# Kernel optimization log

Measured on AMD Instinct MI355X. Metric: run time of the kernel, lower is better.

Reference implementation:

```python
import jax, jax.numpy as jnp
import numpy as np

B, S, D, H = 2, 2048, 1024, 16
DK = D // H

def setup_inputs() -> dict:
    key = jax.random.key(0)
    ks = jax.random.split(key, 11)
    scale = 1.0 / np.sqrt(D)
    inp = {
        'q': jax.random.normal(ks[0], (B, S, D), jnp.float32),
        'k': jax.random.normal(ks[1], (B, S, D), jnp.float32),
        'v': jax.random.normal(ks[2], (B, S, D), jnp.float32),
        'mask': jnp.ones((1, 1, S, S), jnp.int32),
        'Wq': jax.random.normal(ks[3], (D, D), jnp.float32) * scale,
        'bq': jnp.zeros((D,), jnp.float32),
        'Wk': jax.random.normal(ks[4], (D, D), jnp.float32) * scale,
        'bk': jnp.zeros((D,), jnp.float32),
        'Wv': jax.random.normal(ks[5], (D, D), jnp.float32) * scale,
        'bv': jnp.zeros((D,), jnp.float32),
        'Wo': jax.random.normal(ks[6], (D, D), jnp.float32) * scale,
        'bo': jnp.zeros((D,), jnp.float32),
    }
    return inp

def reference(q, k, v, mask, Wq, bq, Wk, bk, Wv, bv, Wo, bo):
    # Linear projections, split into heads: [B,S,D] -> [B,H,S,DK]
    def proj(x, W, b):
        return (x @ W + b).reshape(B, -1, H, DK).transpose(0, 2, 1, 3)
    Q = proj(q, Wq, bq)
    K = proj(k, Wk, bk)
    V = proj(v, Wv, bv)
    scores = jnp.einsum('bhqd,bhkd->bhqk', Q, K) / jnp.sqrt(jnp.float32(DK))
    scores = jnp.where(mask == 0, jnp.float32(-1e9), scores)
    attn = jax.nn.softmax(scores, axis=-1)  # dropout is identity in eval mode
    out = jnp.einsum('bhqk,bhkd->bhqd', attn, V)
    out = out.transpose(0, 2, 1, 3).reshape(B, -1, D)
    return out @ Wo + bo
```

## Files before the change

### kernel.cpp

```cpp
#include <hip/hip_runtime.h>
#include <stdint.h>

#define B_  2
#define S_  2048
#define D_  1024
#define H_  16
#define M_  (B_*S_)

typedef __attribute__((ext_vector_type(8)))  short  short8;
typedef __attribute__((ext_vector_type(4)))  float  floatx4;
typedef __attribute__((ext_vector_type(16))) float  floatx16;
typedef __attribute__((ext_vector_type(4)))  float  f32x4;
typedef __attribute__((ext_vector_type(8)))  unsigned short u16x8;
typedef __attribute__((ext_vector_type(4)))  unsigned short u16x4;
typedef __attribute__((ext_vector_type(2)))  unsigned int   uint2v;

#define LOG2E_  1.44269504088896f
#define QSCALE_ (0.125f * LOG2E_)

#if __has_builtin(__builtin_amdgcn_exp2f)
  #define EXP2(x) __builtin_amdgcn_exp2f(x)
#else
  #define EXP2(x) exp2f(x)
#endif

__device__ __forceinline__ unsigned short f2bf(float x){
  union { float f; uint32_t u; } v; v.f = x;
  uint32_t r = v.u + 0x7FFFu + ((v.u >> 16) & 1u);
  return (unsigned short)(r >> 16);
}

__device__ __forceinline__ uint32_t cvt_pk_bf16(float lo, float hi){
  uint32_t r;
  asm("v_cvt_pk_bf16_f32 %0, %1, %2" : "=v"(r) : "v"(lo), "v"(hi));
  return r;
}

__device__ __forceinline__ void pl32swap(uint32_t &a, uint32_t &b){
#if __has_builtin(__builtin_amdgcn_permlane32_swap)
  uint2v r = __builtin_amdgcn_permlane32_swap(a, b, false, false);
  a = r[0]; b = r[1];
#else
  const int hi = (threadIdx.x & 63) >> 5;
  uint32_t sa = (uint32_t)__shfl_xor((int)a, 32);
  uint32_t sb = (uint32_t)__shfl_xor((int)b, 32);
  uint32_t na = hi ? sb : a;
  uint32_t nb = hi ? b  : sa;
  a = na; b = nb;
#endif
}

#define GLL16(G, L) __builtin_amdgcn_global_load_lds( \
    (const __attribute__((address_space(1))) void*)(G), \
    (__attribute__((address_space(3))) void*)(L), 16, 0, 0)

__global__ __launch_bounds__(256) void k_cvt3(const float* __restrict__ q,
        const float* __restrict__ k, const float* __restrict__ v,
        unsigned short* __restrict__ qb, unsigned short* __restrict__ kb,
        unsigned short* __restrict__ vb){
  const int z = blockIdx.y;
  const float* src = z==0 ? q : z==1 ? k : v;
  unsigned short* dst = z==0 ? qb : z==1 ? kb : vb;
  int i = blockIdx.x*256 + threadIdx.x;
  f32x4 a = ((const f32x4*)src)[i*2];
  f32x4 b = ((const f32x4*)src)[i*2+1];
  u16x8 o;
  o[0]=f2bf(a[0]); o[1]=f2bf(a[1]); o[2]=f2bf(a[2]); o[3]=f2bf(a[3]);
  o[4]=f2bf(b[0]); o[5]=f2bf(b[1]); o[6]=f2bf(b[2]); o[7]=f2bf(b[3]);
  ((u16x8*)dst)[i] = o;
}

__global__ __launch_bounds__(256) void k_wt4(const float* __restrict__ Wq,
        const float* __restrict__ Wk, const float* __restrict__ Wv, const float* __restrict__ Wo,
        unsigned short* __restrict__ wqt, unsigned short* __restrict__ wkt,
        unsigned short* __restrict__ wvt, unsigned short* __restrict__ wot){
  const int z = blockIdx.z;
  const float* W = z==0 ? Wq : z==1 ? Wk : z==2 ? Wv : Wo;
  unsigned short* Wt = z==0 ? wqt : z==1 ? wkt : z==2 ? wvt : wot;
  __shared__ float tile[32][33];
  int n0 = blockIdx.x*32, k0 = blockIdx.y*32;
  int tx = threadIdx.x, ty = threadIdx.y;
  #pragma unroll
  for (int i=0;i<32;i+=8) tile[ty+i][tx] = W[(size_t)(k0+ty+i)*D_ + n0+tx];
  __syncthreads();
  #pragma unroll
  for (int i=0;i<32;i+=8) Wt[(size_t)(n0+ty+i)*D_ + k0+tx] = f2bf(tile[tx][ty+i]);
}

__global__ __launch_bounds__(256) void k_vt64(const unsigned short* __restrict__ Vp,
                                              unsigned short* __restrict__ Vt){
  __shared__ __align__(16) unsigned short t[64*72];
  const int tid = threadIdx.x;
  const int col0 = blockIdx.x*64, row0 = blockIdx.y*64;
  const int b = row0 >> 11, s0 = row0 & 2047;
  #pragma unroll
  for (int it=0; it<2; ++it){
    int i = it*256 + tid;
    int r = i >> 3, c = i & 7;
    short8 v8 = *(const short8*)(Vp + (size_t)(row0 + r)*D_ + col0 + c*8);
    #pragma unroll
    for (int j=0;j<8;j++){
      int d = c*8 + j;
      t[d*72 + (((r>>3) ^ (d&7))*8) + (r&7)] = (unsigned short)v8[j];
    }
  }
  __syncthreads();
  #pragma unroll
  for (int it=0; it<2; ++it){
    int i = it*256 + tid;
    int d = i >> 3, c = i & 7;
    short8 v8 = *(const short8*)(t + d*72 + ((c ^ (d&7))*8));
    *(short8*)(Vt + (size_t)(b*1024 + col0 + d)*S_ + s0 + c*8) = v8;
  }
}

__global__ __launch_bounds__(256) void k_gemm_qkv(
        const unsigned short* __restrict__ qb, const unsigned short* __restrict__ kb,
        const unsigned short* __restrict__ vb,
        const unsigned short* __restrict__ wqt, const unsigned short* __restrict__ wkt,
        const unsigned short* __restrict__ wvt,
        const float* __restrict__ bq, const float* __restrict__ bk, const float* __restrict__ bv,
        unsigned short* __restrict__ Qp, unsigned short* __restrict__ Kp,
        unsigned short* __restrict__ Vp)
{
  __shared__ __align__(16) unsigned short As[128*32];
  __shared__ __align__(16) unsigned short Bs[128*32];
  const int z = blockIdx.z;
  const unsigned short* A  = z==0 ? qb  : z==1 ? kb  : vb;
  const unsigned short* Bt = z==0 ? wqt : z==1 ? wkt : wvt;
  const float* bias        = z==0 ? bq  : z==1 ? bk  : bv;
  unsigned short* C        = z==0 ? Qp  : z==1 ? Kp  : Vp;
  const float scale        = z==0 ? QSCALE_ : 1.0f;

  const int tid = threadIdx.x;
  const int lane = tid & 63, wid = tid >> 6;
  const int wr = wid >> 1, wc = wid & 1;
  const int row0 = blockIdx.y*128, col0 = blockIdx.x*128;
  const int l15 = lane & 15, l4 = lane >> 4;

  floatx4 acc[4][4];
  #pragma unroll
  for (int i=0;i<4;i++)
    #pragma unroll
    for (int j=0;j<4;j++)
      #pragma unroll
      for (int r=0;r<4;r++) acc[i][j][r] = 0.f;

  for (int k0=0; k0<D_; k0+=32){
    __syncthreads();
    #pragma unroll
    for (int it=0; it<2; it++){
      int idx = it*256 + tid;
      int r = idx >> 2, c = idx & 3;
      GLL16(A  + (size_t)(row0 + r)*D_ + k0 + c*8, As + (size_t)(it*4 + wid)*512);
      GLL16(Bt + (size_t)(col0 + r)*D_ + k0 + c*8, Bs + (size_t)(it*4 + wid)*512);
    }
    __syncthreads();
    short8 af[4], bfr[4];
    #pragma unroll
    for (int i=0;i<4;i++)
      af[i] = *(const short8*)(As + (wr*64 + i*16 + l15)*32 + l4*8);
    #pragma unroll
    for (int j=0;j<4;j++)
      bfr[j] = *(const short8*)(Bs + (wc*64 + j*16 + l15)*32 + l4*8);
    #pragma unroll
    for (int i=0;i<4;i++)
      #pragma unroll
      for (int j=0;j<4;j++)
        acc[i][j] = __builtin_amdgcn_mfma_f32_16x16x32_bf16(af[i], bfr[j], acc[i][j], 0,0,0);
  }

  #pragma unroll
  for (int i=0;i<4;i++){
    #pragma unroll
    for (int j=0;j<4;j++){
      int col = col0 + wc*64 + j*16 + l15;
      float bv_ = bias[col];
      int rowb = row0 + wr*64 + i*16 + l4*4;
      #pragma unroll
      for (int r=0;r<4;r++)
        C[(size_t)(rowb + r)*D_ + col] = f2bf((acc[i][j][r] + bv_) * scale);
    }
  }
}

__global__ __launch_bounds__(256) void k_gemm_out(const unsigned short* __restrict__ A,
        const unsigned short* __restrict__ Bt, const float* __restrict__ bias,
        float* __restrict__ C)
{
  __shared__ __align__(16) unsigned short smem[12288];
  unsigned short* const As0 = smem;
  unsigned short* const Bs0 = smem + 2048;
  unsigned short* const As1 = smem + 6144;
  unsigned short* const Bs1 = smem + 8192;

  const int bid = blockIdx.x;
  const int xcd = bid & 7, i2 = bid >> 3;
  const int row0 = (xcd + (i2 >> 3)*8) * 64, col0 = (i2 & 7) * 128;

  const int tid = threadIdx.x;
  const int lane = tid & 63, wid = tid >> 6;
  const int l15 = lane & 15, l4 = lane >> 4;

  floatx4 acc[4][2];
  #pragma unroll
  for (int i=0;i<4;i++)
    #pragma unroll
    for (int j=0;j<2;j++)
      #pragma unroll
      for (int r=0;r<4;r++) acc[i][j][r] = 0.f;

  auto STAGE = [&](unsigned short* As, unsigned short* Bs, int k0){
    #pragma unroll
    for (int it=0; it<2; it++){
      int idx = it*256 + tid;
      int r = idx >> 2, c = idx & 3;
      GLL16(Bt + (size_t)(col0 + r)*D_ + k0 + c*8, Bs + (size_t)(it*4 + wid)*512);
    }
    {
      int r = tid >> 2, c = tid & 3;
      GLL16(A + (size_t)(row0 + r)*D_ + k0 + c*8, As + (size_t)wid*512);
    }
  };
  auto COMPUTE = [&](const unsigned short* As, const unsigned short* Bs){
    short8 af[4], bfr[2];
    #pragma unroll
    for (int i=0;i<4;i++)
      af[i] = *(const short8*)(As + (i*16 + l15)*32 + l4*8);
    #pragma unroll
    for (int j=0;j<2;j++)
      bfr[j] = *(const short8*)(Bs + (wid*32 + j*16 + l15)*32 + l4*8);
    #pragma unroll
    for (int i=0;i<4;i++)
      #pragma unroll
      for (int j=0;j<2;j++)
        acc[i][j] = __builtin_amdgcn_mfma_f32_16x16x32_bf16(af[i], bfr[j], acc[i][j], 0,0,0);
  };

  STAGE(As0, Bs0, 0);
  __syncthreads();
  #pragma unroll 1
  for (int k0=0; k0<D_; k0+=64){
    STAGE(As1, Bs1, k0+32);
    COMPUTE(As0, Bs0);
    __syncthreads();
    if (k0 + 64 < D_) STAGE(As0, Bs0, k0+64);
    COMPUTE(As1, Bs1);
    __syncthreads();
  }

  #pragma unroll
  for (int i=0;i<4;i++){
    #pragma unroll
    for (int j=0;j<2;j++){
      int col = col0 + wid*32 + j*16 + l15;
      float bv_ = bias[col];
      int rowb = row0 + i*16 + l4*4;
      #pragma unroll
      for (int r=0;r<4;r++)
        C[(size_t)(rowb + r)*D_ + col] = acc[i][j][r] + bv_;
    }
  }
}

__global__ __launch_bounds__(256,4) void k_attn(const unsigned short* __restrict__ Qp,
        const unsigned short* __restrict__ Kp, const unsigned short* __restrict__ Vt,
        float* __restrict__ Op, float* __restrict__ Lp)
{
  __shared__ __align__(16) unsigned short smem[16384];
  unsigned short* const kb0 = smem;
  unsigned short* const vb0 = smem + 4096;
  unsigned short* const kb1 = smem + 8192;
  unsigned short* const vb1 = smem + 12288;

  const int sblk = blockIdx.x;
  const int xcd = sblk & 7, jj = sblk >> 3;
  const int bh = xcd + 8*(jj >> 5);
  const int rem = jj & 31, qt = rem >> 1, part = rem & 1;
  const int b = bh >> 4, h = bh & 15;
  const int q0 = qt*128;

  const int tid  = threadIdx.x;
  const int lane = tid & 63, wid = tid >> 6;
  const int lo5  = lane & 31, hi = lane >> 5;
  const int qm = b*S_ + q0 + wid*32 + lo5;

  short8 qf[4];
  #pragma unroll
  for (int f=0; f<4; f++)
    qf[f] = *(const short8*)(Qp + (size_t)qm*D_ + h*64 + f*16 + hi*8);

  floatx16 zv;
  #pragma unroll
  for (int r=0;r<16;r++) zv[r] = 0.f;
  floatx16 ot0 = zv, ot1 = zv;
  float lsum = 0.f;

  const int srow = tid >> 3;
  const int sc   = (tid & 7) ^ (srow & 7);
  const unsigned short* kp0 = Kp + ((size_t)b*S_)*D_ + h*64
                              + (size_t)(part*1024 + srow)*D_ + sc*8;
  const unsigned short* kp1 = kp0 + (size_t)32*D_;
  const unsigned short* vp0 = Vt + ((size_t)(b*1024 + h*64 + srow))*S_ + part*1024 + sc*8;
  const unsigned short* vp1 = vp0 + (size_t)32*S_;

  auto STAGE = [&](unsigned short* kdst, unsigned short* vdst, int tt){
    const size_t ko = (size_t)tt*64*D_;
    const int    vo = tt*64;
    GLL16(kp0 + ko, kdst + wid*512);
    GLL16(kp1 + ko, kdst + (4+wid)*512);
    GLL16(vp0 + vo, vdst + wid*512);
    GLL16(vp1 + vo, vdst + (4+wid)*512);
  };

  const int ksw = lo5 & 7;

  auto COMPUTE = [&](const unsigned short* kbuf, const unsigned short* vbuf){
    floatx16 st0, st1;
    __builtin_amdgcn_s_setprio(1);
    {
      const int cc = hi ^ ksw;
      short8 ka0 = *(const short8*)(kbuf + lo5*64      + cc*8);
      short8 ka1 = *(const short8*)(kbuf + (32+lo5)*64 + cc*8);
      st0 = __builtin_amdgcn_mfma_f32_32x32x16_bf16(ka0, qf[0], zv, 0,0,0);
      st1 = __builtin_amdgcn_mfma_f32_32x32x16_bf16(ka1, qf[0], zv, 0,0,0);
    }
    #pragma unroll
    for (int f=1; f<4; f++){
      const int cc = (2*f + hi) ^ ksw;
      short8 ka0 = *(const short8*)(kbuf + lo5*64      + cc*8);
      short8 ka1 = *(const short8*)(kbuf + (32+lo5)*64 + cc*8);
      st0 = __builtin_amdgcn_mfma_f32_32x32x16_bf16(ka0, qf[f], st0, 0,0,0);
      st1 = __builtin_amdgcn_mfma_f32_32x32x16_bf16(ka1, qf[f], st1, 0,0,0);
    }
    __builtin_amdgcn_s_setprio(0);

    #pragma unroll
    for (int kh=0; kh<2; kh++){
      const floatx16& st = kh ? st1 : st0;
      #pragma unroll
      for (int blk=0; blk<2; blk++){
        const int bs = blk*8;
        float e0 = EXP2(st[bs+0]), e1 = EXP2(st[bs+1]);
        float e2 = EXP2(st[bs+2]), e3 = EXP2(st[bs+3]);
        float e4 = EXP2(st[bs+4]), e5 = EXP2(st[bs+5]);
        float e6 = EXP2(st[bs+6]), e7 = EXP2(st[bs+7]);
        lsum += ((e0+e1)+(e2+e3)) + ((e4+e5)+(e6+e7));
        uint32_t a01 = cvt_pk_bf16(e0,e1);
        uint32_t a23 = cvt_pk_bf16(e2,e3);
        uint32_t a45 = cvt_pk_bf16(e4,e5);
        uint32_t a67 = cvt_pk_bf16(e6,e7);
        pl32swap(a01, a45);
        pl32swap(a23, a67);
        union { uint32_t w[4]; short8 v; } pu;
        pu.w[0] = a01; pu.w[1] = a23; pu.w[2] = a45; pu.w[3] = a67;
        const int kvc = kh*4 + blk*2 + hi;
        {
          const int d = lo5;
          short8 va = *(const short8*)(vbuf + d*64 + ((kvc ^ (d&7))*8));
          ot0 = __builtin_amdgcn_mfma_f32_32x32x16_bf16(va, pu.v, ot0, 0,0,0);
        }
        {
          const int d = 32 + lo5;
          short8 va = *(const short8*)(vbuf + d*64 + ((kvc ^ (d&7))*8));
          ot1 = __builtin_amdgcn_mfma_f32_32x32x16_bf16(va, pu.v, ot1, 0,0,0);
        }
      }
    }
  };

  STAGE(kb0, vb0, 0);
  __syncthreads();
  #pragma unroll 1
  for (int t2=0; t2<8; ++t2){
    const int tt = t2*2;
    STAGE(kb1, vb1, tt+1);
    COMPUTE(kb0, vb0);
    __syncthreads();
    if (t2 < 7) STAGE(kb0, vb0, tt+2);
    COMPUTE(kb1, vb1);
    __syncthreads();
  }

  lsum += __shfl_xor(lsum, 32);
  if (hi == 0)
    Lp[(size_t)part*65536 + (size_t)h*4096 + qm] = lsum;

  float* ob = Op + ((size_t)part << 22);
  #pragma unroll
  for (int r=0;r<16;r++){
    const int d = (r&3) + 8*(r>>2) + 4*hi;
    ob[(size_t)(h*64 + d)*4096      + qm] = ot0[r];
    ob[(size_t)(h*64 + d + 32)*4096 + qm] = ot1[r];
  }
}

__global__ __launch_bounds__(256) void k_combine(const float* __restrict__ Op,
        const float* __restrict__ Lp, unsigned short* __restrict__ Of)
{
  __shared__ float tile[64*68];
  __shared__ float linv[64];
  const int bx = blockIdx.x;
  const int mt = bx & 63, h = bx >> 6;
  const int m0 = mt*64, d0 = h*64;
  const int t = threadIdx.x;

  if (t < 64){
    float l0 = Lp[(size_t)h*4096 + m0 + t];
    float l1 = Lp[65536 + (size_t)h*4096 + m0 + t];
    linv[t] = 1.0f / (l0 + l1);
  }
  __syncthreads();

  const int dd = t >> 2, mc = t & 3;
  const float* p0 = Op + (size_t)(d0 + dd)*4096 + m0 + mc*16;
  const float* p1 = p0 + 4194304;
  #pragma unroll
  for (int i=0;i<4;i++){
    f32x4 a = *(const f32x4*)(p0 + i*4);
    f32x4 bb = *(const f32x4*)(p1 + i*4);
    f32x4 iv = *(const f32x4*)(linv + mc*16 + i*4);
    f32x4 vv = (a + bb) * iv;
    *(f32x4*)(tile + dd*68 + mc*16 + i*4) = vv;
  }
  __syncthreads();

  const int mm = t >> 2, dc = t & 3;
  u16x8 o0, o1;
  #pragma unroll
  for (int j=0;j<8;j++) o0[j] = f2bf(tile[(dc*16 + j)*68 + mm]);
  #pragma unroll
  for (int j=0;j<8;j++) o1[j] = f2bf(tile[(dc*16 + 8 + j)*68 + mm]);
  *(u16x8*)(Of + (size_t)(m0 + mm)*1024 + d0 + dc*16)     = o0;
  *(u16x8*)(Of + (size_t)(m0 + mm)*1024 + d0 + dc*16 + 8) = o1;
}

extern "C" void kernel_launch(void* const* d_in, const int* in_sizes, int n_in,
                              void* d_out, int out_size, void* d_ws, size_t ws_size,
                              hipStream_t stream)
{
  (void)in_sizes; (void)n_in; (void)out_size; (void)ws_size;
  const float* q  = (const float*)d_in[0];
  const float* k  = (const float*)d_in[1];
  const float* v  = (const float*)d_in[2];
  const float* Wq = (const float*)d_in[4];
  const float* bq = (const float*)d_in[5];
  const float* Wk = (const float*)d_in[6];
  const float* bk = (const float*)d_in[7];
  const float* Wv = (const float*)d_in[8];
  const float* bv = (const float*)d_in[9];
  const float* Wo = (const float*)d_in[10];
  const float* bo = (const float*)d_in[11];

  char* ws = (char*)d_ws;
  unsigned short* Qp  = (unsigned short*)(ws + 0);
  unsigned short* Kp  = (unsigned short*)(ws + 8388608);
  unsigned short* Vt  = (unsigned short*)(ws + 16777216);
  unsigned short* qb  = (unsigned short*)(ws + 25165824);
  unsigned short* kb  = (unsigned short*)(ws + 33554432);
  unsigned short* vb  = (unsigned short*)(ws + 41943040);
  unsigned short* wqt = (unsigned short*)(ws + 50331648);
  unsigned short* wkt = (unsigned short*)(ws + 52428800);
  unsigned short* wvt = (unsigned short*)(ws + 54525952);
  unsigned short* Vp  = (unsigned short*)(ws + 56623104);
  unsigned short* wot = (unsigned short*)(ws + 67108864);
  float*          Lp  = (float*)         (ws + 69206016);
  float*          Op  = (float*)         (ws + 33554432);
  unsigned short* Of  = qb;

  const int n8 = M_*D_/8;
  k_cvt3<<<dim3(n8/256, 3), 256, 0, stream>>>(q, k, v, qb, kb, vb);
  k_wt4<<<dim3(D_/32, D_/32, 4), dim3(32,8), 0, stream>>>(Wq, Wk, Wv, Wo,
                                                          wqt, wkt, wvt, wot);

  k_gemm_qkv<<<dim3(D_/128, M_/128, 3), 256, 0, stream>>>(qb, kb, vb, wqt, wkt, wvt,
                                                          bq, bk, bv, Qp, Kp, Vp);

  k_vt64<<<dim3(D_/64, M_/64), 256, 0, stream>>>(Vp, Vt);

  k_attn<<<dim3(1024), 256, 0, stream>>>(Qp, Kp, Vt, Op, Lp);

  k_combine<<<dim3(1024), 256, 0, stream>>>(Op, Lp, Of);

  k_gemm_out<<<dim3(512), 256, 0, stream>>>(Of, wot, bo, (float*)d_out);
}
```

Measured before the change: 130.8 us.

## Merge prep kernels, double-buffer QKV GEMM, split attention KV into four bf16 partials

The input conversion and weight transpose kernels are merged into one launch, which removes a kernel launch. The QKV GEMM now uses double-buffered LDS so the next k-tile loads while MFMAs run on the current one. Attention splits the key range into four parts instead of two, doubling the grid for more parallelism, and stores its partial outputs as bf16 to cut write and read traffic. The combine kernel sums the four partials, which adds a bf16 rounding step on unnormalized partial sums and more Lp reads.

```diff
diff --git a/kernel.cpp b/kernel.cpp
--- a/kernel.cpp
+++ b/kernel.cpp
@@ -28,6 +28,9 @@
   union { float f; uint32_t u; } v; v.f = x;
   uint32_t r = v.u + 0x7FFFu + ((v.u >> 16) & 1u);
   return (unsigned short)(r >> 16);
+}
+__device__ __forceinline__ float bf2f(unsigned short u){
+  union { uint32_t i; float f; } v; v.i = ((uint32_t)u) << 16; return v.f;
 }
 
 __device__ __forceinline__ uint32_t cvt_pk_bf16(float lo, float hi){
@@ -54,37 +57,41 @@
     (const __attribute__((address_space(1))) void*)(G), \
     (__attribute__((address_space(3))) void*)(L), 16, 0, 0)
 
-__global__ __launch_bounds__(256) void k_cvt3(const float* __restrict__ q,
-        const float* __restrict__ k, const float* __restrict__ v,
+__global__ __launch_bounds__(256) void k_prep(
+        const float* __restrict__ q, const float* __restrict__ k, const float* __restrict__ v,
+        const float* __restrict__ Wq, const float* __restrict__ Wk,
+        const float* __restrict__ Wv, const float* __restrict__ Wo,
         unsigned short* __restrict__ qb, unsigned short* __restrict__ kb,
-        unsigned short* __restrict__ vb){
-  const int z = blockIdx.y;
-  const float* src = z==0 ? q : z==1 ? k : v;
-  unsigned short* dst = z==0 ? qb : z==1 ? kb : vb;
-  int i = blockIdx.x*256 + threadIdx.x;
-  f32x4 a = ((const f32x4*)src)[i*2];
-  f32x4 b = ((const f32x4*)src)[i*2+1];
-  u16x8 o;
-  o[0]=f2bf(a[0]); o[1]=f2bf(a[1]); o[2]=f2bf(a[2]); o[3]=f2bf(a[3]);
-  o[4]=f2bf(b[0]); o[5]=f2bf(b[1]); o[6]=f2bf(b[2]); o[7]=f2bf(b[3]);
-  ((u16x8*)dst)[i] = o;
-}
-
-__global__ __launch_bounds__(256) void k_wt4(const float* __restrict__ Wq,
-        const float* __restrict__ Wk, const float* __restrict__ Wv, const float* __restrict__ Wo,
+        unsigned short* __restrict__ vb,
         unsigned short* __restrict__ wqt, unsigned short* __restrict__ wkt,
-        unsigned short* __restrict__ wvt, unsigned short* __restrict__ wot){
-  const int z = blockIdx.z;
-  const float* W = z==0 ? Wq : z==1 ? Wk : z==2 ? Wv : Wo;
-  unsigned short* Wt = z==0 ? wqt : z==1 ? wkt : z==2 ? wvt : wot;
+        unsigned short* __restrict__ wvt, unsigned short* __restrict__ wot)
+{
   __shared__ float tile[32][33];
-  int n0 = blockIdx.x*32, k0 = blockIdx.y*32;
-  int tx = threadIdx.x, ty = threadIdx.y;
-  #pragma unroll
-  for (int i=0;i<32;i+=8) tile[ty+i][tx] = W[(size_t)(k0+ty+i)*D_ + n0+tx];
-  __syncthreads();
-  #pragma unroll
-  for (int i=0;i<32;i+=8) Wt[(size_t)(n0+ty+i)*D_ + k0+tx] = f2bf(tile[tx][ty+i]);
+  const int bid = blockIdx.x, tid = threadIdx.x;
+  if (bid < 6144){
+    const int z = bid >> 11, ib = bid & 2047;
+    const float* src = z==0 ? q : z==1 ? k : v;
+    unsigned short* dst = z==0 ? qb : z==1 ? kb : vb;
+    int i = ib*256 + tid;
+    f32x4 a = ((const f32x4*)src)[i*2];
+    f32x4 b = ((const f32x4*)src)[i*2+1];
+    u16x8 o;
+    o[0]=f2bf(a[0]); o[1]=f2bf(a[1]); o[2]=f2bf(a[2]); o[3]=f2bf(a[3]);
+    o[4]=f2bf(b[0]); o[5]=f2bf(b[1]); o[6]=f2bf(b[2]); o[7]=f2bf(b[3]);
+    ((u16x8*)dst)[i] = o;
+  } else {
+    const int wb = bid - 6144;
+    const int z = wb >> 10, t2 = wb & 1023;
+    const float* W = z==0 ? Wq : z==1 ? Wk : z==2 ? Wv : Wo;
+    unsigned short* Wt = z==0 ? wqt : z==1 ? wkt : z==2 ? wvt : wot;
+    const int n0 = (t2 & 31)*32, k0 = (t2 >> 5)*32;
+    const int tx = tid & 31, ty = tid >> 5;
+    #pragma unroll
+    for (int i=0;i<32;i+=8) tile[ty+i][tx] = W[(size_t)(k0+ty+i)*D_ + n0+tx];
+    __syncthreads();
+    #pragma unroll
+    for (int i=0;i<32;i+=8) Wt[(size_t)(n0+ty+i)*D_ + k0+tx] = f2bf(tile[tx][ty+i]);
+  }
 }
 
 __global__ __launch_bounds__(256) void k_vt64(const unsigned short* __restrict__ Vp,
@@ -123,8 +130,12 @@
         unsigned short* __restrict__ Qp, unsigned short* __restrict__ Kp,
         unsigned short* __restrict__ Vp)
 {
-  __shared__ __align__(16) unsigned short As[128*32];
-  __shared__ __align__(16) unsigned short Bs[128*32];
+  __shared__ __align__(16) unsigned short smem[16384];
+  unsigned short* const As0 = smem;
+  unsigned short* const Bs0 = smem + 4096;
+  unsigned short* const As1 = smem + 8192;
+  unsigned short* const Bs1 = smem + 12288;
+
   const int z = blockIdx.z;
   const unsigned short* A  = z==0 ? qb  : z==1 ? kb  : vb;
   const unsigned short* Bt = z==0 ? wqt : z==1 ? wkt : wvt;
@@ -146,8 +157,7 @@
       #pragma unroll
       for (int r=0;r<4;r++) acc[i][j][r] = 0.f;
 
-  for (int k0=0; k0<D_; k0+=32){
-    __syncthreads();
+  auto STAGE = [&](unsigned short* As, unsigned short* Bs, int k0){
     #pragma unroll
     for (int it=0; it<2; it++){
       int idx = it*256 + tid;
@@ -155,7 +165,8 @@
       GLL16(A  + (size_t)(row0 + r)*D_ + k0 + c*8, As + (size_t)(it*4 + wid)*512);
       GLL16(Bt + (size_t)(col0 + r)*D_ + k0 + c*8, Bs + (size_t)(it*4 + wid)*512);
     }
-    __syncthreads();
+  };
+  auto COMPUTE = [&](const unsigned short* As, const unsigned short* Bs){
     short8 af[4], bfr[4];
     #pragma unroll
     for (int i=0;i<4;i++)
@@ -168,6 +179,18 @@
       #pragma unroll
       for (int j=0;j<4;j++)
         acc[i][j] = __builtin_amdgcn_mfma_f32_16x16x32_bf16(af[i], bfr[j], acc[i][j], 0,0,0);
+  };
+
+  STAGE(As0, Bs0, 0);
+  __syncthreads();
+  #pragma unroll 1
+  for (int k0=0; k0<D_; k0+=64){
+    STAGE(As1, Bs1, k0+32);
+    COMPUTE(As0, Bs0);
+    __syncthreads();
+    if (k0 + 64 < D_) STAGE(As0, Bs0, k0+64);
+    COMPUTE(As1, Bs1);
+    __syncthreads();
   }
 
   #pragma unroll
@@ -265,7 +288,7 @@
 
 __global__ __launch_bounds__(256,4) void k_attn(const unsigned short* __restrict__ Qp,
         const unsigned short* __restrict__ Kp, const unsigned short* __restrict__ Vt,
-        float* __restrict__ Op, float* __restrict__ Lp)
+        unsigned short* __restrict__ Opb, float* __restrict__ Lp)
 {
   __shared__ __align__(16) unsigned short smem[16384];
   unsigned short* const kb0 = smem;
@@ -275,8 +298,8 @@
 
   const int sblk = blockIdx.x;
   const int xcd = sblk & 7, jj = sblk >> 3;
-  const int bh = xcd + 8*(jj >> 5);
-  const int rem = jj & 31, qt = rem >> 1, part = rem & 1;
+  const int bh = xcd + 8*(jj >> 6);
+  const int rem = jj & 63, qt = rem >> 2, part = rem & 3;
   const int b = bh >> 4, h = bh & 15;
   const int q0 = qt*128;
 
@@ -299,9 +322,9 @@
   const int srow = tid >> 3;
   const int sc   = (tid & 7) ^ (srow & 7);
   const unsigned short* kp0 = Kp + ((size_t)b*S_)*D_ + h*64
-                              + (size_t)(part*1024 + srow)*D_ + sc*8;
+                              + (size_t)(part*512 + srow)*D_ + sc*8;
   const unsigned short* kp1 = kp0 + (size_t)32*D_;
-  const unsigned short* vp0 = Vt + ((size_t)(b*1024 + h*64 + srow))*S_ + part*1024 + sc*8;
+  const unsigned short* vp0 = Vt + ((size_t)(b*1024 + h*64 + srow))*S_ + part*512 + sc*8;
   const unsigned short* vp1 = vp0 + (size_t)32*S_;
 
   auto STAGE = [&](unsigned short* kdst, unsigned short* vdst, int tt){
@@ -372,12 +395,12 @@
   STAGE(kb0, vb0, 0);
   __syncthreads();
   #pragma unroll 1
-  for (int t2=0; t2<8; ++t2){
+  for (int t2=0; t2<4; ++t2){
     const int tt = t2*2;
     STAGE(kb1, vb1, tt+1);
     COMPUTE(kb0, vb0);
     __syncthreads();
-    if (t2 < 7) STAGE(kb0, vb0, tt+2);
+    if (t2 < 3) STAGE(kb0, vb0, tt+2);
     COMPUTE(kb1, vb1);
     __syncthreads();
   }
@@ -386,16 +409,16 @@
   if (hi == 0)
     Lp[(size_t)part*65536 + (size_t)h*4096 + qm] = lsum;
 
-  float* ob = Op + ((size_t)part << 22);
+  unsigned short* ob = Opb + ((size_t)part << 22);
   #pragma unroll
   for (int r=0;r<16;r++){
     const int d = (r&3) + 8*(r>>2) + 4*hi;
-    ob[(size_t)(h*64 + d)*4096      + qm] = ot0[r];
-    ob[(size_t)(h*64 + d + 32)*4096 + qm] = ot1[r];
-  }
-}
-
-__global__ __launch_bounds__(256) void k_combine(const float* __restrict__ Op,
+    ob[(size_t)(h*64 + d)*4096      + qm] = f2bf(ot0[r]);
+    ob[(size_t)(h*64 + d + 32)*4096 + qm] = f2bf(ot1[r]);
+  }
+}
+
+__global__ __launch_bounds__(256) void k_combine(const unsigned short* __restrict__ Opb,
         const float* __restrict__ Lp, unsigned short* __restrict__ Of)
 {
   __shared__ float tile[64*68];
@@ -406,23 +429,27 @@
   const int t = threadIdx.x;
 
   if (t < 64){
-    float l0 = Lp[(size_t)h*4096 + m0 + t];
-    float l1 = Lp[65536 + (size_t)h*4096 + m0 + t];
-    linv[t] = 1.0f / (l0 + l1);
+    float l = 0.f;
+    #pragma unroll
+    for (int p=0;p<4;p++) l += Lp[(size_t)p*65536 + (size_t)h*4096 + m0 + t];
+    linv[t] = 1.0f / l;
   }
   __syncthreads();
 
   const int dd = t >> 2, mc = t & 3;
-  const float* p0 = Op + (size_t)(d0 + dd)*4096 + m0 + mc*16;
-  const float* p1 = p0 + 4194304;
-  #pragma unroll
-  for (int i=0;i<4;i++){
-    f32x4 a = *(const f32x4*)(p0 + i*4);
-    f32x4 bb = *(const f32x4*)(p1 + i*4);
-    f32x4 iv = *(const f32x4*)(linv + mc*16 + i*4);
-    f32x4 vv = (a + bb) * iv;
-    *(f32x4*)(tile + dd*68 + mc*16 + i*4) = vv;
-  }
+  float s[16];
+  #pragma unroll
+  for (int j=0;j<16;j++) s[j] = 0.f;
+  #pragma unroll
+  for (int p=0;p<4;p++){
+    const unsigned short* pp = Opb + ((size_t)p << 22) + (size_t)(d0 + dd)*4096 + m0 + mc*16;
+    u16x8 a = *(const u16x8*)pp;
+    u16x8 b = *(const u16x8*)(pp + 8);
+    #pragma unroll
+    for (int j=0;j<8;j++){ s[j] += bf2f(a[j]); s[8+j] += bf2f(b[j]); }
+  }
+  #pragma unroll
+  for (int j=0;j<16;j++) tile[dd*68 + mc*16 + j] = s[j] * linv[mc*16 + j];
   __syncthreads();
 
   const int mm = t >> 2, dc = t & 3;
@@ -464,23 +491,21 @@
   unsigned short* wvt = (unsigned short*)(ws + 54525952);
   unsigned short* Vp  = (unsigned short*)(ws + 56623104);
   unsigned short* wot = (unsigned short*)(ws + 67108864);
-  float*          Lp  = (float*)         (ws + 69206016);
-  float*          Op  = (float*)         (ws + 33554432);
-  unsigned short* Of  = qb;
-
-  const int n8 = M_*D_/8;
-  k_cvt3<<<dim3(n8/256, 3), 256, 0, stream>>>(q, k, v, qb, kb, vb);
-  k_wt4<<<dim3(D_/32, D_/32, 4), dim3(32,8), 0, stream>>>(Wq, Wk, Wv, Wo,
-                                                          wqt, wkt, wvt, wot);
+  float*          Lp  = (float*)         (ws + 25165824);
+  unsigned short* Opb = (unsigned short*)(ws + 33554432);
+  unsigned short* Of  = Qp;
+
+  k_prep<<<dim3(10240), 256, 0, stream>>>(q, k, v, Wq, Wk, Wv, Wo,
+                                          qb, kb, vb, wqt, wkt, wvt, wot);
 
   k_gemm_qkv<<<dim3(D_/128, M_/128, 3), 256, 0, stream>>>(qb, kb, vb, wqt, wkt, wvt,
                                                           bq, bk, bv, Qp, Kp, Vp);
 
   k_vt64<<<dim3(D_/64, M_/64), 256, 0, stream>>>(Vp, Vt);
 
-  k_attn<<<dim3(1024), 256, 0, stream>>>(Qp, Kp, Vt, Op, Lp);
-
-  k_combine<<<dim3(1024), 256, 0, stream>>>(Op, Lp, Of);
+  k_attn<<<dim3(2048), 256, 0, stream>>>(Qp, Kp, Vt, Opb, Lp);
+
+  k_combine<<<dim3(1024), 256, 0, stream>>>(Opb, Lp, Of);
 
   k_gemm_out<<<dim3(512), 256, 0, stream>>>(Of, wot, bo, (float*)d_out);
 }
```

New measurement: 130.5 us. No clear change (-0.3%).
